# Optimization experiments

Measured on AMD Instinct MI355X. Metric: run time of the kernel, lower is better.

Reference implementation:

```python
import jax, jax.numpy as jnp
import numpy as np

D_IN_NUM = 16
D_IN_CAT = 16
D_OUT = 10
DIM = 512
N_FREQ = 32
FREQ_SCALE = 0.01
D_EMB = 48
TEMP = 1.0
CHUNK = 5000


def setup_inputs() -> dict:
    key = jax.random.key(0)
    ks = jax.random.split(key, 10)
    B, N = 1024, 40000
    d_in_total = D_IN_NUM * D_EMB + D_IN_CAT
    return {
        "x_num": jax.random.uniform(ks[0], (B, D_IN_NUM), dtype=jnp.float32),
        "x_cat": jax.random.uniform(ks[1], (B, D_IN_CAT), dtype=jnp.float32),
        "y": jax.random.randint(ks[2], (B,), 0, D_OUT),
        "candidate_x_num": jax.random.uniform(ks[3], (N, D_IN_NUM), dtype=jnp.float32),
        "candidate_x_cat": jax.random.uniform(ks[4], (N, D_IN_CAT), dtype=jnp.float32),
        "candidate_y": jax.random.randint(ks[5], (N,), 0, D_OUT),
        "frequencies": FREQ_SCALE * jax.random.normal(ks[6], (D_IN_NUM, N_FREQ), dtype=jnp.float32),
        "lin_w": 0.05 * jax.random.normal(ks[7], (2 * N_FREQ, D_EMB), dtype=jnp.float32),
        "lin_b": jnp.zeros((D_EMB,), dtype=jnp.float32),
        "enc_w": 0.02 * jax.random.normal(ks[8], (d_in_total, DIM), dtype=jnp.float32),
        "enc_b": jnp.zeros((DIM,), dtype=jnp.float32),
    }


def _plr_encode(x_num, x_cat, frequencies, lin_w, lin_b, enc_w, enc_b):
    # PLR 'lite' embedding: [B, F] -> [B, F, 2*n_freq] -> [B, F, d_emb]
    t = 2.0 * jnp.pi * frequencies[None] * x_num[:, :, None]        # [B,F,n_freq]
    feats = jnp.concatenate([jnp.cos(t), jnp.sin(t)], axis=-1)       # [B,F,2n_freq]
    emb = jax.nn.relu(feats @ lin_w + lin_b)                         # [B,F,d_emb]
    flat = emb.reshape(emb.shape[0], -1)                             # [B,F*d_emb]
    h = jnp.concatenate([flat, x_cat], axis=1) @ enc_w + enc_b       # [B,dim]
    return h


def reference(x_num, x_cat, y, candidate_x_num, candidate_x_cat, candidate_y,
              frequencies, lin_w, lin_b, enc_w, enc_b):
    q = _plr_encode(x_num, x_cat, frequencies, lin_w, lin_b, enc_w, enc_b)           # [B,dim]
    c = _plr_encode(candidate_x_num, candidate_x_cat, frequencies, lin_w, lin_b, enc_w, enc_b)  # [N,dim]
    cand_y = jax.nn.one_hot(candidate_y, D_OUT, dtype=jnp.float32)                   # [N,K]

    # pairwise Euclidean distance (matmul form, as torch.cdist)
    d2 = (jnp.sum(q * q, axis=1, keepdims=True)
          + jnp.sum(c * c, axis=1)[None, :]
          - 2.0 * q @ c.T)
    dist = jnp.sqrt(jnp.maximum(d2, 1e-12)) / TEMP                                   # [B,N]
    exp_d = jnp.exp(-dist)                                                           # [B,N]

    # original accumulates per-5000-chunk logsumexp of exp(-d) additively
    B, N = exp_d.shape
    n_chunks = N // CHUNK
    lse = jax.nn.logsumexp(exp_d.reshape(B, n_chunks, CHUNK), axis=-1).sum(axis=-1)  # [B]
    logits = exp_d @ cand_y                                                          # [B,K]
    return jnp.log(logits) - lse[:, None]
```

## Files before the change

### kernel.cpp

```cpp
#include <hip/hip_runtime.h>
#include <math.h>

typedef __attribute__((ext_vector_type(8))) short bf16x8;
typedef __attribute__((ext_vector_type(4))) float f32x4;
typedef unsigned short u16;
typedef unsigned int u32;

#define BQ 1024
#define NCAND 40000
#define ROWS_TOT 41024
#define NF 16
#define NFREQ 32
#define DEMB 48
#define KDIM 800
#define ASTRIDE 808
#define DIM 512
#define NCLS 10
#define NCHUNK 8
#define CHUNKSZ 5000
#define CT_PER_CHUNK 40
#define NCT 320
#define PSTRIDE 136
#define MROWS 64
#define TWO_PI 6.28318530717958647692f

__device__ __forceinline__ u16 f2bf(float f) {
  u32 u = __float_as_uint(f);
  u32 r = u + 0x7fffu + ((u >> 16) & 1u);
  return (u16)(r >> 16);
}
__device__ __forceinline__ float bf2f(u16 b) { return __uint_as_float(((u32)b) << 16); }
__device__ __forceinline__ u32 cvt_pk_bf16(float lo, float hi) {
  u32 r;
  asm("v_cvt_pk_bf16_f32 %0, %1, %2" : "=v"(r) : "v"(lo), "v"(hi));
  return r;
}

__global__ __launch_bounds__(256)
void k_prep(const float* __restrict__ enc_w, u16* __restrict__ enc_wT)
{
  int idx = blockIdx.x * 256 + threadIdx.x;
  if (idx >= DIM * KDIM) return;
  int n = idx / KDIM, k = idx - n * KDIM;
  u16 v = 0;
  if (k < 784) v = f2bf(enc_w[k * DIM + n]);
  enc_wT[idx] = v;
}

__global__ __launch_bounds__(512, 2)
void k_encode(const float* __restrict__ xq_num, const float* __restrict__ xq_cat,
              const float* __restrict__ xc_num, const float* __restrict__ xc_cat,
              const float* __restrict__ freq, const float* __restrict__ lin_w,
              const float* __restrict__ lin_b, const u16* __restrict__ enc_wT,
              const float* __restrict__ enc_b,
              u16* __restrict__ h_bf, float* __restrict__ norms)
{
  __shared__ u16 a_s[MROWS * ASTRIDE];
  __shared__ float norm_s[MROWS];

  const int t = threadIdx.x;
  const int row0 = blockIdx.x * MROWS;
  const bool isq = (row0 < BQ);
  const float* __restrict__ xnum = isq ? xq_num : xc_num;
  const float* __restrict__ xcat = isq ? xq_cat : xc_cat;
  const int rbase = isq ? row0 : (row0 - BQ);

  const int wid = t >> 6, l = t & 63, hi = l >> 4, lo = l & 15;

  if (t < MROWS) norm_s[t] = 0.f;
  for (int i = t; i < MROWS * 16; i += 512) {
    int r = i >> 4, c = i & 15;
    a_s[r * ASTRIDE + 768 + c] = f2bf(xcat[(rbase + r) * NF + c]);
  }
  for (int i = t; i < MROWS * 24; i += 512) {
    int r = i / 24, c = i - r * 24;
    a_s[r * ASTRIDE + 784 + c] = 0;
  }

  {
    float fq[8];
    *(float4*)&fq[0] = *(const float4*)&freq[lo * NFREQ + hi * 8];
    *(float4*)&fq[4] = *(const float4*)&freq[lo * NFREQ + hi * 8 + 4];
    float xv[8];
#pragma unroll
    for (int mi = 0; mi < 8; ++mi)
      xv[mi] = xnum[(rbase + wid * 8 + mi) * NF + lo];

    bf16x8 lwb[2][3];
#pragma unroll
    for (int kf = 0; kf < 2; ++kf)
#pragma unroll
      for (int nf = 0; nf < 3; ++nf)
#pragma unroll
        for (int e = 0; e < 8; ++e)
          lwb[kf][nf][e] = (short)f2bf(lin_w[(kf * 32 + hi * 8 + e) * DEMB + nf * 16 + lo]);
    float lb[3];
#pragma unroll
    for (int nf = 0; nf < 3; ++nf) lb[nf] = lin_b[nf * 16 + lo];

#pragma unroll
    for (int mi = 0; mi < 8; ++mi) {
      bf16x8 ac, as_;
#pragma unroll
      for (int e = 0; e < 8; ++e) {
        float tt = TWO_PI * fq[e] * xv[mi];
        ac[e] = (short)f2bf(__cosf(tt));
        as_[e] = (short)f2bf(__sinf(tt));
      }
#pragma unroll
      for (int nf = 0; nf < 3; ++nf) {
        f32x4 ec = {0.f, 0.f, 0.f, 0.f};
        ec = __builtin_amdgcn_mfma_f32_16x16x32_bf16(ac, lwb[0][nf], ec, 0, 0, 0);
        ec = __builtin_amdgcn_mfma_f32_16x16x32_bf16(as_, lwb[1][nf], ec, 0, 0, 0);
#pragma unroll
        for (int reg = 0; reg < 4; ++reg) {
          int f = hi * 4 + reg;
          int r = wid * 8 + mi;
          float v = fmaxf(ec[reg] + lb[nf], 0.f);
          a_s[r * ASTRIDE + f * DEMB + nf * 16 + lo] = f2bf(v);
        }
      }
    }
  }
  __syncthreads();

  f32x4 acc[4][4];
#pragma unroll
  for (int mf = 0; mf < 4; ++mf)
#pragma unroll
    for (int nf = 0; nf < 4; ++nf) acc[mf][nf] = 0.f;

  const u16* bwbase = enc_wT + (size_t)(wid * 64 + lo) * KDIM + hi * 8;
  const u16* asbase = a_s + lo * ASTRIDE + hi * 8;

  bf16x8 afA[4], bwA[4], afB[4], bwB[4];

#define LOADK(kt, af, bw)                                                     \
  {                                                                           \
    _Pragma("unroll")                                                         \
    for (int nf = 0; nf < 4; ++nf)                                            \
      bw[nf] = *(const bf16x8*)(bwbase + (size_t)nf * 16 * KDIM + (kt) * 32); \
    _Pragma("unroll")                                                         \
    for (int mf = 0; mf < 4; ++mf)                                            \
      af[mf] = *(const bf16x8*)(asbase + mf * 16 * ASTRIDE + (kt) * 32);      \
  }
#define MFMAK(af, bw)                                                         \
  {                                                                           \
    _Pragma("unroll")                                                         \
    for (int mf = 0; mf < 4; ++mf)                                            \
      _Pragma("unroll")                                                       \
      for (int nf = 0; nf < 4; ++nf)                                          \
        acc[mf][nf] =                                                         \
            __builtin_amdgcn_mfma_f32_16x16x32_bf16(af[mf], bw[nf],           \
                                                    acc[mf][nf], 0, 0, 0);    \
  }

  LOADK(0, afA, bwA);
#pragma unroll
  for (int i = 0; i < 12; ++i) {
    LOADK(2 * i + 1, afB, bwB);
    MFMAK(afA, bwA);
    LOADK(2 * i + 2, afA, bwA);
    MFMAK(afB, bwB);
  }
  MFMAK(afA, bwA);
#undef LOADK
#undef MFMAK

  float encb_v[4];
#pragma unroll
  for (int nf = 0; nf < 4; ++nf) encb_v[nf] = enc_b[wid * 64 + nf * 16 + lo];
  float nacc[4][4];
#pragma unroll
  for (int mf = 0; mf < 4; ++mf)
#pragma unroll
    for (int r = 0; r < 4; ++r) nacc[mf][r] = 0.f;

#pragma unroll
  for (int mf = 0; mf < 4; ++mf)
#pragma unroll
    for (int nf = 0; nf < 4; ++nf)
#pragma unroll
      for (int r = 0; r < 4; ++r) {
        int m = mf * 16 + hi * 4 + r;
        int n = wid * 64 + nf * 16 + lo;
        float hv = acc[mf][nf][r] + encb_v[nf];
        u16 ub = f2bf(hv);
        h_bf[(size_t)(row0 + m) * DIM + n] = ub;
        float hb = bf2f(ub);
        nacc[mf][r] = fmaf(hb, hb, nacc[mf][r]);
      }
#pragma unroll
  for (int mf = 0; mf < 4; ++mf)
#pragma unroll
    for (int r = 0; r < 4; ++r) {
      float v = nacc[mf][r];
      v += __shfl_xor(v, 1); v += __shfl_xor(v, 2);
      v += __shfl_xor(v, 4); v += __shfl_xor(v, 8);
      if (lo == 0) atomicAdd(&norm_s[mf * 16 + hi * 4 + r], v);
    }
  __syncthreads();
  if (t < MROWS) norms[row0 + t] = norm_s[t];
}

__global__ __launch_bounds__(256)
void k_dist(const u16* __restrict__ h_bf, const float* __restrict__ norms,
            const int* __restrict__ cand_y,
            float* __restrict__ cls_part, float* __restrict__ lse_part)
{
  __shared__ __align__(16) u16 AB_s[12288];
  __shared__ float qn_s[64];
  __shared__ float cn_s[128];
  __shared__ int cy_s[128];
  __shared__ float lse_s[64];

  u16* A_s = AB_s;
  u16* B_s = AB_s + 8192;
  u16* P_s = AB_s;

  const int t = threadIdx.x;
  const int bx = blockIdx.x;
  const int chunk = bx / CT_PER_CHUNK;
  const int ctl = bx - chunk * CT_PER_CHUNK;
  const int cand0 = chunk * CHUNKSZ + ctl * 128;
  const int cend = chunk * CHUNKSZ + CHUNKSZ;
  const int q0 = blockIdx.y * 64;

  if (t < 64) { lse_s[t] = 0.f; qn_s[t] = norms[q0 + t]; }
  if (t < 128) {
    int j = cand0 + t; if (j > cend - 1) j = cend - 1;
    cn_s[t] = norms[BQ + j];
    cy_s[t] = cand_y[j];
  }

  const int wid = t >> 6, l = t & 63, hi = l >> 4, lo = l & 15;
  const int wm = wid & 1, wn = wid >> 1;

  f32x4 acc[4][2];
#pragma unroll
  for (int mi = 0; mi < 4; ++mi)
#pragma unroll
    for (int ni = 0; ni < 2; ++ni) acc[mi][ni] = 0.f;

  for (int kt = 0; kt < DIM / 64; ++kt) {
    __syncthreads();
#pragma unroll
    for (int p = 0; p < 4; ++p) {
      int idx = p * 256 + t;
      int lrow = idx >> 3, slot = idx & 7;
      int crow = cand0 + lrow; if (crow > cend - 1) crow = cend - 1;
      float4 v = *(const float4*)&h_bf[(size_t)(BQ + crow) * DIM + kt * 64 + slot * 8];
      *(float4*)&A_s[lrow * 64 + ((((u32)slot * 16) ^ (((u32)lrow & 7) << 4)) >> 1)] = v;
    }
#pragma unroll
    for (int p = 0; p < 2; ++p) {
      int idx = p * 256 + t;
      int qrow = idx >> 3, slot = idx & 7;
      float4 v = *(const float4*)&h_bf[(size_t)(q0 + qrow) * DIM + kt * 64 + slot * 8];
      *(float4*)&B_s[qrow * 64 + ((((u32)slot * 16) ^ (((u32)qrow & 7) << 4)) >> 1)] = v;
    }
    __syncthreads();
#pragma unroll
    for (int ks = 0; ks < 2; ++ks) {
      bf16x8 af[4], bq[2];
#pragma unroll
      for (int mi = 0; mi < 4; ++mi) {
        int row = wm * 64 + mi * 16 + lo;
        int byt = (hi * 16 + ks * 64) ^ ((row & 7) << 4);
        af[mi] = *(const bf16x8*)&A_s[row * 64 + (byt >> 1)];
      }
#pragma unroll
      for (int ni = 0; ni < 2; ++ni) {
        int row = wn * 32 + ni * 16 + lo;
        int byt = (hi * 16 + ks * 64) ^ ((row & 7) << 4);
        bq[ni] = *(const bf16x8*)&B_s[row * 64 + (byt >> 1)];
      }
#pragma unroll
      for (int mi = 0; mi < 4; ++mi)
#pragma unroll
        for (int ni = 0; ni < 2; ++ni)
          acc[mi][ni] = __builtin_amdgcn_mfma_f32_16x16x32_bf16(af[mi], bq[ni], acc[mi][ni], 0, 0, 0);
    }
  }

  float qv[2];
#pragma unroll
  for (int ni = 0; ni < 2; ++ni) qv[ni] = qn_s[wn * 32 + ni * 16 + lo];

  u32 pk[4][2][2];
  float lacc[2] = {0.f, 0.f};
#pragma unroll
  for (int mi = 0; mi < 4; ++mi)
#pragma unroll
    for (int ni = 0; ni < 2; ++ni) {
      float ev[4];
#pragma unroll
      for (int r = 0; r < 4; ++r) {
        int crow = wm * 64 + mi * 16 + hi * 4 + r;
        bool valid = (cand0 + crow) < cend;
        float d2 = fmaf(-2.f, acc[mi][ni][r], cn_s[crow] + qv[ni]);
        float dist = __builtin_amdgcn_sqrtf(fmaxf(d2, 1e-12f));
        float e = valid ? __expf(-dist) : 0.f;
        ev[r] = e;
        lacc[ni] += valid ? __expf(e) : 0.f;
      }
      pk[mi][ni][0] = cvt_pk_bf16(ev[0], ev[1]);
      pk[mi][ni][1] = cvt_pk_bf16(ev[2], ev[3]);
    }

#pragma unroll
  for (int ni = 0; ni < 2; ++ni) {
    float v = lacc[ni];
    v += __shfl_xor(v, 16); v += __shfl_xor(v, 32);
    if (hi == 0) atomicAdd(&lse_s[wn * 32 + ni * 16 + lo], v);
  }

  __syncthreads();
#pragma unroll
  for (int mi = 0; mi < 4; ++mi)
#pragma unroll
    for (int ni = 0; ni < 2; ++ni) {
      int q = wn * 32 + ni * 16 + lo;
      int j0 = wm * 64 + mi * 16 + hi * 4;
      *(uint2*)&P_s[q * PSTRIDE + j0] = make_uint2(pk[mi][ni][0], pk[mi][ni][1]);
    }
  __syncthreads();

  {
    f32x4 accc = {0.f, 0.f, 0.f, 0.f};
    const u16* Prow = P_s + (wn * 32 + wm * 16 + lo) * PSTRIDE;
#pragma unroll
    for (int ks = 0; ks < 4; ++ks) {
      bf16x8 af = *(const bf16x8*)(Prow + ks * 32 + hi * 8);
      bf16x8 yb;
#pragma unroll
      for (int e = 0; e < 8; ++e) {
        int j = ks * 32 + hi * 8 + e;
        yb[e] = (short)((cy_s[j] == lo) ? 0x3F80 : 0);
      }
      accc = __builtin_amdgcn_mfma_f32_16x16x32_bf16(af, yb, accc, 0, 0, 0);
    }
    if (lo < NCLS) {
#pragma unroll
      for (int reg = 0; reg < 4; ++reg) {
        int qq = wn * 32 + wm * 16 + hi * 4 + reg;
        cls_part[((size_t)bx * BQ + (q0 + qq)) * NCLS + lo] = accc[reg];
      }
    }
  }

  if (t < 64) lse_part[(size_t)bx * BQ + q0 + t] = lse_s[t];
}

__global__ __launch_bounds__(320)
void k_final(const float* __restrict__ cls_part, const float* __restrict__ lse_part,
             float* __restrict__ out)
{
  __shared__ float cls_sum[NCLS];
  __shared__ float ch_sum[NCHUNK];
  const int t = threadIdx.x;
  const int b = blockIdx.x;
  if (t < NCLS) cls_sum[t] = 0.f;
  if (t < NCHUNK) ch_sum[t] = 0.f;
  __syncthreads();

  float cs[NCLS];
#pragma unroll
  for (int c = 0; c < NCLS; ++c) cs[c] = cls_part[((size_t)t * BQ + b) * NCLS + c];
  float ls = lse_part[(size_t)t * BQ + b];
  atomicAdd(&ch_sum[t / CT_PER_CHUNK], ls);
#pragma unroll
  for (int c = 0; c < NCLS; ++c) {
    float w = cs[c];
    w += __shfl_xor(w, 1); w += __shfl_xor(w, 2); w += __shfl_xor(w, 4);
    w += __shfl_xor(w, 8); w += __shfl_xor(w, 16); w += __shfl_xor(w, 32);
    if ((t & 63) == 0) atomicAdd(&cls_sum[c], w);
  }
  __syncthreads();
  if (t < NCLS) {
    float lse = 0.f;
#pragma unroll
    for (int ch = 0; ch < NCHUNK; ++ch) lse += logf(ch_sum[ch]);
    out[b * NCLS + t] = logf(cls_sum[t]) - lse;
  }
}

extern "C" void kernel_launch(void* const* d_in, const int* in_sizes, int n_in,
                              void* d_out, int out_size, void* d_ws, size_t ws_size,
                              hipStream_t stream)
{
  const float* xq_num = (const float*)d_in[0];
  const float* xq_cat = (const float*)d_in[1];
  const float* xc_num = (const float*)d_in[3];
  const float* xc_cat = (const float*)d_in[4];
  const int* cand_y = (const int*)d_in[5];
  const float* freq = (const float*)d_in[6];
  const float* lin_w = (const float*)d_in[7];
  const float* lin_b = (const float*)d_in[8];
  const float* enc_w = (const float*)d_in[9];
  const float* enc_b = (const float*)d_in[10];

  u16* h_bf = (u16*)d_ws;
  float* norms = (float*)((char*)d_ws + (size_t)ROWS_TOT * DIM * 2);
  float* cls_part = norms + ROWS_TOT;
  float* lse_part = cls_part + (size_t)NCT * BQ * NCLS;
  u16* enc_wT = (u16*)(lse_part + (size_t)NCT * BQ);
  float* out = (float*)d_out;

  hipLaunchKernelGGL(k_prep, dim3((DIM * KDIM + 255) / 256), dim3(256), 0, stream,
                     enc_w, enc_wT);
  hipLaunchKernelGGL(k_encode, dim3(ROWS_TOT / MROWS), dim3(512), 0, stream,
                     xq_num, xq_cat, xc_num, xc_cat, freq, lin_w, lin_b,
                     enc_wT, enc_b, h_bf, norms);
  hipLaunchKernelGGL(k_dist, dim3(NCT, BQ / 64), dim3(256), 0, stream,
                     h_bf, norms, cand_y, cls_part, lse_part);
  hipLaunchKernelGGL(k_final, dim3(BQ), dim3(320), 0, stream,
                     cls_part, lse_part, out);
}
```

Measured before the change: 188.8 us.

## Enlarge distance tile to 128x128 with double-buffered direct global-to-LDS loads

The distance kernel's query tile grows from 64 to 128 rows, so each block computes a 128x128 tile with a 4x4 MFMA accumulator per wave. Operand staging now uses global_load_lds direct copies into two LDS buffers, prefetching the next K slice while the current one is computed. The grid is transposed so neighbouring blocks share a candidate tile across query tiles. The aim is to raise arithmetic intensity, hide global load latency and drop one barrier per K step. In exchange it uses more LDS (64KB) and more accumulator registers, which can lower occupancy.

```diff
diff --git a/kernel.cpp b/kernel.cpp
--- a/kernel.cpp
+++ b/kernel.cpp
@@ -208,95 +208,108 @@
             const int* __restrict__ cand_y,
             float* __restrict__ cls_part, float* __restrict__ lse_part)
 {
-  __shared__ __align__(16) u16 AB_s[12288];
-  __shared__ float qn_s[64];
+  __shared__ __align__(16) u16 AB_s[32768];
+  __shared__ float qn_s[128];
   __shared__ float cn_s[128];
   __shared__ int cy_s[128];
-  __shared__ float lse_s[64];
-
-  u16* A_s = AB_s;
-  u16* B_s = AB_s + 8192;
+  __shared__ float lse_s[128];
+
   u16* P_s = AB_s;
 
   const int t = threadIdx.x;
-  const int bx = blockIdx.x;
-  const int chunk = bx / CT_PER_CHUNK;
-  const int ctl = bx - chunk * CT_PER_CHUNK;
+  const int by = blockIdx.y;
+  const int chunk = by / CT_PER_CHUNK;
+  const int ctl = by - chunk * CT_PER_CHUNK;
   const int cand0 = chunk * CHUNKSZ + ctl * 128;
   const int cend = chunk * CHUNKSZ + CHUNKSZ;
-  const int q0 = blockIdx.y * 64;
-
-  if (t < 64) { lse_s[t] = 0.f; qn_s[t] = norms[q0 + t]; }
+  const int q0 = blockIdx.x * 128;
+
   if (t < 128) {
+    lse_s[t] = 0.f;
+    qn_s[t] = norms[q0 + t];
     int j = cand0 + t; if (j > cend - 1) j = cend - 1;
     cn_s[t] = norms[BQ + j];
     cy_s[t] = cand_y[j];
   }
 
   const int wid = t >> 6, l = t & 63, hi = l >> 4, lo = l & 15;
-  const int wm = wid & 1, wn = wid >> 1;
-
-  f32x4 acc[4][2];
+  const int wc = wid & 1, wq = wid >> 1;
+
+#define STAGE(dstoff, kt)                                                      \
+  {                                                                            \
+    _Pragma("unroll")                                                          \
+    for (int p = 0; p < 4; ++p) {                                              \
+      int seg = wid * 4 + p;                                                   \
+      int lrow = seg * 8 + (l >> 3);                                           \
+      int scol = ((l & 7) * 16) ^ ((lrow & 7) << 4);                           \
+      int crow = cand0 + lrow; if (crow > cend - 1) crow = cend - 1;           \
+      const u16* srcA = h_bf + (size_t)(BQ + crow) * DIM + (kt) * 64 + (scol >> 1); \
+      __builtin_amdgcn_global_load_lds(                                        \
+          (const __attribute__((address_space(1))) u32*)srcA,                  \
+          (__attribute__((address_space(3))) u32*)(AB_s + (dstoff) + seg * 512), \
+          16, 0, 0);                                                           \
+      const u16* srcB = h_bf + (size_t)(q0 + lrow) * DIM + (kt) * 64 + (scol >> 1); \
+      __builtin_amdgcn_global_load_lds(                                        \
+          (const __attribute__((address_space(1))) u32*)srcB,                  \
+          (__attribute__((address_space(3))) u32*)(AB_s + (dstoff) + 8192 + seg * 512), \
+          16, 0, 0);                                                           \
+    }                                                                          \
+  }
+
+  f32x4 acc[4][4];
 #pragma unroll
   for (int mi = 0; mi < 4; ++mi)
 #pragma unroll
-    for (int ni = 0; ni < 2; ++ni) acc[mi][ni] = 0.f;
-
+    for (int ni = 0; ni < 4; ++ni) acc[mi][ni] = 0.f;
+
+  STAGE(0, 0);
+  __syncthreads();
+
+  int cur = 0;
   for (int kt = 0; kt < DIM / 64; ++kt) {
+    if (kt < DIM / 64 - 1) STAGE((cur ^ 1) * 16384, kt + 1);
+    const u16* Ac = AB_s + cur * 16384;
+    const u16* Bc = Ac + 8192;
+#pragma unroll
+    for (int ks = 0; ks < 2; ++ks) {
+      bf16x8 af[4], bq[4];
+#pragma unroll
+      for (int mi = 0; mi < 4; ++mi) {
+        int row = wc * 64 + mi * 16 + lo;
+        int byt = (hi * 16 + ks * 64) ^ ((row & 7) << 4);
+        af[mi] = *(const bf16x8*)&Ac[row * 64 + (byt >> 1)];
+      }
+#pragma unroll
+      for (int ni = 0; ni < 4; ++ni) {
+        int row = wq * 64 + ni * 16 + lo;
+        int byt = (hi * 16 + ks * 64) ^ ((row & 7) << 4);
+        bq[ni] = *(const bf16x8*)&Bc[row * 64 + (byt >> 1)];
+      }
+#pragma unroll
+      for (int mi = 0; mi < 4; ++mi)
+#pragma unroll
+        for (int ni = 0; ni < 4; ++ni)
+          acc[mi][ni] = __builtin_amdgcn_mfma_f32_16x16x32_bf16(af[mi], bq[ni], acc[mi][ni], 0, 0, 0);
+    }
     __syncthreads();
-#pragma unroll
-    for (int p = 0; p < 4; ++p) {
-      int idx = p * 256 + t;
-      int lrow = idx >> 3, slot = idx & 7;
-      int crow = cand0 + lrow; if (crow > cend - 1) crow = cend - 1;
-      float4 v = *(const float4*)&h_bf[(size_t)(BQ + crow) * DIM + kt * 64 + slot * 8];
-      *(float4*)&A_s[lrow * 64 + ((((u32)slot * 16) ^ (((u32)lrow & 7) << 4)) >> 1)] = v;
-    }
-#pragma unroll
-    for (int p = 0; p < 2; ++p) {
-      int idx = p * 256 + t;
-      int qrow = idx >> 3, slot = idx & 7;
-      float4 v = *(const float4*)&h_bf[(size_t)(q0 + qrow) * DIM + kt * 64 + slot * 8];
-      *(float4*)&B_s[qrow * 64 + ((((u32)slot * 16) ^ (((u32)qrow & 7) << 4)) >> 1)] = v;
-    }
-    __syncthreads();
-#pragma unroll
-    for (int ks = 0; ks < 2; ++ks) {
-      bf16x8 af[4], bq[2];
-#pragma unroll
-      for (int mi = 0; mi < 4; ++mi) {
-        int row = wm * 64 + mi * 16 + lo;
-        int byt = (hi * 16 + ks * 64) ^ ((row & 7) << 4);
-        af[mi] = *(const bf16x8*)&A_s[row * 64 + (byt >> 1)];
-      }
-#pragma unroll
-      for (int ni = 0; ni < 2; ++ni) {
-        int row = wn * 32 + ni * 16 + lo;
-        int byt = (hi * 16 + ks * 64) ^ ((row & 7) << 4);
-        bq[ni] = *(const bf16x8*)&B_s[row * 64 + (byt >> 1)];
-      }
-#pragma unroll
-      for (int mi = 0; mi < 4; ++mi)
-#pragma unroll
-        for (int ni = 0; ni < 2; ++ni)
-          acc[mi][ni] = __builtin_amdgcn_mfma_f32_16x16x32_bf16(af[mi], bq[ni], acc[mi][ni], 0, 0, 0);
-    }
-  }
-
-  float qv[2];
-#pragma unroll
-  for (int ni = 0; ni < 2; ++ni) qv[ni] = qn_s[wn * 32 + ni * 16 + lo];
-
-  u32 pk[4][2][2];
-  float lacc[2] = {0.f, 0.f};
+    cur ^= 1;
+  }
+#undef STAGE
+
+  float qv[4];
+#pragma unroll
+  for (int ni = 0; ni < 4; ++ni) qv[ni] = qn_s[wq * 64 + ni * 16 + lo];
+
+  u32 pk[4][4][2];
+  float lacc[4] = {0.f, 0.f, 0.f, 0.f};
 #pragma unroll
   for (int mi = 0; mi < 4; ++mi)
 #pragma unroll
-    for (int ni = 0; ni < 2; ++ni) {
+    for (int ni = 0; ni < 4; ++ni) {
       float ev[4];
 #pragma unroll
       for (int r = 0; r < 4; ++r) {
-        int crow = wm * 64 + mi * 16 + hi * 4 + r;
+        int crow = wc * 64 + mi * 16 + hi * 4 + r;
         bool valid = (cand0 + crow) < cend;
         float d2 = fmaf(-2.f, acc[mi][ni][r], cn_s[crow] + qv[ni]);
         float dist = __builtin_amdgcn_sqrtf(fmaxf(d2, 1e-12f));
@@ -309,26 +322,27 @@
     }
 
 #pragma unroll
-  for (int ni = 0; ni < 2; ++ni) {
+  for (int ni = 0; ni < 4; ++ni) {
     float v = lacc[ni];
     v += __shfl_xor(v, 16); v += __shfl_xor(v, 32);
-    if (hi == 0) atomicAdd(&lse_s[wn * 32 + ni * 16 + lo], v);
+    if (hi == 0) atomicAdd(&lse_s[wq * 64 + ni * 16 + lo], v);
   }
 
   __syncthreads();
 #pragma unroll
   for (int mi = 0; mi < 4; ++mi)
 #pragma unroll
-    for (int ni = 0; ni < 2; ++ni) {
-      int q = wn * 32 + ni * 16 + lo;
-      int j0 = wm * 64 + mi * 16 + hi * 4;
+    for (int ni = 0; ni < 4; ++ni) {
+      int q = wq * 64 + ni * 16 + lo;
+      int j0 = wc * 64 + mi * 16 + hi * 4;
       *(uint2*)&P_s[q * PSTRIDE + j0] = make_uint2(pk[mi][ni][0], pk[mi][ni][1]);
     }
   __syncthreads();
 
-  {
+#pragma unroll
+  for (int g = 0; g < 2; ++g) {
     f32x4 accc = {0.f, 0.f, 0.f, 0.f};
-    const u16* Prow = P_s + (wn * 32 + wm * 16 + lo) * PSTRIDE;
+    const u16* Prow = P_s + (wid * 32 + g * 16 + lo) * PSTRIDE;
 #pragma unroll
     for (int ks = 0; ks < 4; ++ks) {
       bf16x8 af = *(const bf16x8*)(Prow + ks * 32 + hi * 8);
@@ -343,13 +357,13 @@
     if (lo < NCLS) {
 #pragma unroll
       for (int reg = 0; reg < 4; ++reg) {
-        int qq = wn * 32 + wm * 16 + hi * 4 + reg;
-        cls_part[((size_t)bx * BQ + (q0 + qq)) * NCLS + lo] = accc[reg];
-      }
-    }
-  }
-
-  if (t < 64) lse_part[(size_t)bx * BQ + q0 + t] = lse_s[t];
+        int qq = wid * 32 + g * 16 + hi * 4 + reg;
+        cls_part[((size_t)by * BQ + (q0 + qq)) * NCLS + lo] = accc[reg];
+      }
+    }
+  }
+
+  if (t < 128) lse_part[(size_t)by * BQ + q0 + t] = lse_s[t];
 }
 
 __global__ __launch_bounds__(320)
@@ -412,7 +426,7 @@
   hipLaunchKernelGGL(k_encode, dim3(ROWS_TOT / MROWS), dim3(512), 0, stream,
                      xq_num, xq_cat, xc_num, xc_cat, freq, lin_w, lin_b,
                      enc_wT, enc_b, h_bf, norms);
-  hipLaunchKernelGGL(k_dist, dim3(NCT, BQ / 64), dim3(256), 0, stream,
+  hipLaunchKernelGGL(k_dist, dim3(BQ / 128, NCT), dim3(256), 0, stream,
                      h_bf, norms, cand_y, cls_part, lse_part);
   hipLaunchKernelGGL(k_final, dim3(BQ), dim3(320), 0, stream,
                      cls_part, lse_part, out);
```

Measured after the change: 192.0 us. No clear change (+1.7%).
